# Kernel tuning notes

Measured on AMD Instinct MI355X. Metric: run time of the kernel, lower is better.

Reference implementation:

```python
import jax, jax.numpy as jnp
import numpy as np

D = 1024      # in_dim
HS = 64       # head_size
H = 16        # num_heads
B, S = 2, 2048


def setup_inputs() -> dict:
    key = jax.random.key(0)
    k1, k2, k3, k4, k5, k6 = jax.random.split(key, 6)
    scale = 1.0 / np.sqrt(D)
    x = jax.random.normal(k1, (B, S, D), dtype=jnp.float32)
    # Stacked per-head projection weights (torch Linear weight is [out,in];
    # random init so layout only needs to be consistent). query weight exists
    # in the torch module but is never used (source bug), so it is omitted.
    Wk = jax.random.normal(k2, (H, D, HS), dtype=jnp.float32) * scale
    Wv = jax.random.normal(k3, (H, D, HS), dtype=jnp.float32) * scale
    Wproj = jax.random.normal(k4, (H * HS, D), dtype=jnp.float32) * (1.0 / np.sqrt(H * HS))
    bproj = jax.random.normal(k5, (D,), dtype=jnp.float32) * 0.01
    return {"x": x, "Wk": Wk, "Wv": Wv, "Wproj": Wproj, "bproj": bproj}


def reference(x, Wk, Wv, Wproj, bproj):
    # Faithful to source: k = key(x); q = value(x); v = value(x)  (q == v, no softmax)
    k = jnp.einsum("bsd,hde->bhse", x, Wk)   # [B,H,S,HS]
    v = jnp.einsum("bsd,hde->bhse", x, Wv)   # [B,H,S,HS]
    q = v
    inv_sqrt = jnp.asarray(HS, x.dtype) ** -0.5
    wei = jnp.einsum("bhse,bhte->bhst", q, k) * inv_sqrt  # [B,H,S,S], unnormalized
    out = jnp.einsum("bhst,bhte->bhse", wei, v)            # [B,H,S,HS]
    # concat heads: [B,S,H*HS]
    out = jnp.transpose(out, (0, 2, 1, 3)).reshape(x.shape[0], x.shape[1], H * HS)
    return out @ Wproj + bproj  # [B,S,D]
```

## Files before the change

kernel.cpp:

```cpp
#include <hip/hip_runtime.h>

#define B_ 2
#define S_ 2048
#define D_ 1024
#define H_ 16
#define HS_ 64
#define HD_ 1024
#define BS_ (B_*S_)
#define KS_ 64
#define TP2_ 264

typedef __attribute__((ext_vector_type(8))) short short8_t;
typedef __attribute__((ext_vector_type(4))) float float4_t;

__device__ inline unsigned short f32_to_bf16(float f) {
  unsigned int u = __float_as_uint(f);
  u += 0x7FFF + ((u >> 16) & 1);
  return (unsigned short)(u >> 16);
}

__device__ inline void async_copy16(const void* g, void* lds) {
  __builtin_amdgcn_global_load_lds(
      (const __attribute__((address_space(1))) void*)g,
      (__attribute__((address_space(3))) void*)lds, 16, 0, 0);
}


__global__ __launch_bounds__(256) void prep_kernel(
    const float* __restrict__ x, const float* __restrict__ Wk,
    const float* __restrict__ Wv, unsigned short* __restrict__ xb,
    unsigned short* __restrict__ Wkvt) {
  const int blk = blockIdx.x;
  const int tid = threadIdx.x;
  __shared__ float lds[64][65];
  if (blk < 4096) {
    int idx = blk * 256 + tid;
    float4 v = ((const float4*)x)[idx];
    ushort4 o;
    o.x = f32_to_bf16(v.x); o.y = f32_to_bf16(v.y);
    o.z = f32_to_bf16(v.z); o.w = f32_to_bf16(v.w);
    ((ushort4*)xb)[idx] = o;
    return;
  }
  const int wblk = blk - 4096;
  const int h = wblk >> 4;
  const int d0 = (wblk & 15) * 64;
#pragma unroll
  for (int i = 0; i < 16; ++i) {
    int idx = tid + i * 256; int dd = idx >> 6, e = idx & 63;
    lds[e][dd] = Wk[((size_t)h * D_ + d0 + dd) * HS_ + e];
  }
  __syncthreads();
#pragma unroll
  for (int i = 0; i < 16; ++i) {
    int idx = tid + i * 256; int e = idx >> 6, dd = idx & 63;
    Wkvt[((size_t)h * 128 + e) * D_ + d0 + dd] = f32_to_bf16(lds[e][dd]);
  }
  __syncthreads();
#pragma unroll
  for (int i = 0; i < 16; ++i) {
    int idx = tid + i * 256; int dd = idx >> 6, e = idx & 63;
    lds[e][dd] = Wv[((size_t)h * D_ + d0 + dd) * HS_ + e];
  }
  __syncthreads();
#pragma unroll
  for (int i = 0; i < 16; ++i) {
    int idx = tid + i * 256; int e = idx >> 6, dd = idx & 63;
    Wkvt[((size_t)h * 128 + 64 + e) * D_ + d0 + dd] = f32_to_bf16(lds[e][dd]);
  }
}

__global__ __launch_bounds__(512) void kv_mfma_kernel(
    const unsigned short* __restrict__ xb,
    const unsigned short* __restrict__ Wkvt,
    unsigned short* __restrict__ Vb,
    float* __restrict__ Mpart) {
  const int blk = blockIdx.x;
  const int stile = blk & 15;
  const int h = blk >> 4;
  const int s0 = stile * 256;
  const int tid = threadIdx.x;
  const int lane = tid & 63;
  const int wid = tid >> 6;
  const int wm = wid >> 1, wn = wid & 1;
  const int quad = lane >> 4, l16 = lane & 15;
  const int srow8 = lane >> 3;
  const int sc8 = lane & 7;
  const int xa = l16 & 7;

  __shared__ __align__(16) unsigned char smem[98304];
  unsigned short* const A0 = (unsigned short*)smem;
  unsigned short* const B0 = (unsigned short*)(smem + 32768);
  unsigned short* const A1 = (unsigned short*)(smem + 49152);
  unsigned short* const B1 = (unsigned short*)(smem + 81920);
  unsigned short* const Ktl = (unsigned short*)smem;
  unsigned short* const Vtl = (unsigned short*)(smem + 64 * TP2_ * 2);

  float4_t acc[4][4];
  const float4_t fz = {0.f, 0.f, 0.f, 0.f};
#pragma unroll
  for (int i = 0; i < 4; ++i)
#pragma unroll
    for (int j = 0; j < 4; ++j) acc[i][j] = fz;

  auto stage_half = [&](int kt, unsigned short* Ad, unsigned short* Bd, int hf) {
    const int k0 = kt * KS_;
#pragma unroll
    for (int i = 0; i < 2; ++i) {
      int g = wid * 4 + hf * 2 + i;
      int r = g * 8 + srow8;
      int ch = (sc8 ^ (r & 7)) * 8;
      async_copy16(xb + (size_t)(s0 + r) * D_ + k0 + ch, Ad + g * 8 * KS_);
    }
    {
      int g = wid * 2 + hf;
      int r = g * 8 + srow8;
      int ch = (sc8 ^ (r & 7)) * 8;
      async_copy16(Wkvt + ((size_t)h * 128 + r) * D_ + k0 + ch, Bd + g * 8 * KS_);
    }
  };
  auto compute_phase = [&](const unsigned short* Ac, const unsigned short* Bc,
                           int ks) {
    short8_t a[4], b[4];
#pragma unroll
    for (int mi = 0; mi < 4; ++mi)
      a[mi] = *(const short8_t*)(Ac + (wm * 64 + mi * 16 + l16) * KS_ +
                                 ((ks * 4 + quad) ^ xa) * 8);
#pragma unroll
    for (int ni = 0; ni < 4; ++ni)
      b[ni] = *(const short8_t*)(Bc + (wn * 64 + ni * 16 + l16) * KS_ +
                                 ((ks * 4 + quad) ^ xa) * 8);
    __builtin_amdgcn_s_setprio(1);
#pragma unroll
    for (int mi = 0; mi < 4; ++mi)
#pragma unroll
      for (int ni = 0; ni < 4; ++ni)
        acc[mi][ni] = __builtin_amdgcn_mfma_f32_16x16x32_bf16(
            a[mi], b[ni], acc[mi][ni], 0, 0, 0);
    __builtin_amdgcn_s_setprio(0);
  };

  stage_half(0, A0, B0, 0);
  stage_half(0, A0, B0, 1);
  for (int t = 0; t < 16; ++t) {
    unsigned short* Ac = (t & 1) ? A1 : A0;
    unsigned short* Bc = (t & 1) ? B1 : B0;
    unsigned short* An = (t & 1) ? A0 : A1;
    unsigned short* Bn = (t & 1) ? B0 : B1;
    if (t < 15) {
      stage_half(t + 1, An, Bn, 0);
      asm volatile("s_waitcnt vmcnt(3)" ::: "memory");
    } else {
      asm volatile("s_waitcnt vmcnt(0)" ::: "memory");
    }
    __builtin_amdgcn_s_barrier();
    __builtin_amdgcn_sched_barrier(0);
    compute_phase(Ac, Bc, 0);
    __builtin_amdgcn_sched_barrier(0);
    __builtin_amdgcn_s_barrier();
    if (t < 15) stage_half(t + 1, An, Bn, 1);
    __builtin_amdgcn_s_barrier();
    __builtin_amdgcn_sched_barrier(0);
    compute_phase(Ac, Bc, 1);
    __builtin_amdgcn_sched_barrier(0);
    __builtin_amdgcn_s_barrier();
  }

  {
    unsigned short* dstT = (wn == 0) ? Ktl : Vtl;
#pragma unroll
    for (int mi = 0; mi < 4; ++mi)
#pragma unroll
      for (int ni = 0; ni < 4; ++ni) {
        int f = ni * 16 + l16;
        int sm = wm * 64 + mi * 16 + quad * 4;
        ushort4 o;
        o.x = f32_to_bf16(acc[mi][ni][0]);
        o.y = f32_to_bf16(acc[mi][ni][1]);
        o.z = f32_to_bf16(acc[mi][ni][2]);
        o.w = f32_to_bf16(acc[mi][ni][3]);
        *(ushort4*)&dstT[f * TP2_ + sm] = o;
      }
  }
  __syncthreads();

#pragma unroll
  for (int u = 0; u < 4; ++u) {
    int unit = tid + u * 512;
    int s = unit & 255;
    int ec = (unit >> 8) * 8;
    union { unsigned short u16[8]; uint4 v; } tv;
#pragma unroll
    for (int e = 0; e < 8; ++e) tv.u16[e] = Vtl[(ec + e) * TP2_ + s];
    *(uint4*)&Vb[(size_t)(s0 + s) * HD_ + h * 64 + ec] = tv.v;
  }

  {
    const int half = wid >> 2, fq = wid & 3;
    float4_t macc[4];
#pragma unroll
    for (int ni = 0; ni < 4; ++ni) macc[ni] = fz;
#pragma unroll
    for (int ss = 0; ss < 4; ++ss) {
      short8_t ka = *(const short8_t*)&Ktl[(fq * 16 + l16) * TP2_ +
                                           half * 128 + ss * 32 + quad * 8];
#pragma unroll
      for (int ni = 0; ni < 4; ++ni) {
        short8_t vv = *(const short8_t*)&Vtl[(ni * 16 + l16) * TP2_ +
                                             half * 128 + ss * 32 + quad * 8];
        macc[ni] = __builtin_amdgcn_mfma_f32_16x16x32_bf16(ka, vv, macc[ni], 0, 0, 0);
      }
    }
    float* mdst = Mpart + (((size_t)(stile * 2 + half)) * H_ + h) * 4096;
#pragma unroll
    for (int ni = 0; ni < 4; ++ni) {
      int e = ni * 16 + l16;
#pragma unroll
      for (int r = 0; r < 4; ++r) {
        int f = fq * 16 + quad * 4 + r;
        mdst[f * 64 + e] = macc[ni][r];
      }
    }
  }
}

__global__ __launch_bounds__(256) void m_reduce_kernel(
    const float* __restrict__ Mpart, float* __restrict__ M) {
  const int gid = blockIdx.x * 256 + threadIdx.x;
  const int e0 = gid * 4;
  const int bh = e0 >> 12;
  const int idx = e0 & 4095;
  const int b = bh >> 4, h = bh & 15;
  float4 s = {0.f, 0.f, 0.f, 0.f};
#pragma unroll
  for (int p = 0; p < 16; ++p) {
    const float4 v =
        *(const float4*)&Mpart[(((size_t)(b * 16 + p)) * H_ + h) * 4096 + idx];
    s.x += v.x; s.y += v.y; s.z += v.z; s.w += v.w;
  }
  s.x *= 0.125f; s.y *= 0.125f; s.z *= 0.125f; s.w *= 0.125f;
  *(float4*)&M[(size_t)bh * 4096 + idx] = s;
}

__global__ __launch_bounds__(256) void p_kernel(
    const float* __restrict__ M, const float* __restrict__ Wproj,
    unsigned short* __restrict__ Pt) {
  const int blk = blockIdx.x;
  const int dtile = blk & 15;
  const int h = (blk >> 4) & 15;
  const int b = blk >> 8;
  const int d0 = dtile * 64;
  const int tid = threadIdx.x;
  const int tx = tid & 15, ty = tid >> 4;
  __shared__ float Ms[64][68];
  __shared__ float Ws[64][68];
  const size_t mbase = ((size_t)(b * H_ + h)) * HS_ * HS_;
#pragma unroll
  for (int i = 0; i < 16; ++i) {
    int idx = tid + i * 256;
    int f = idx >> 6, e = idx & 63;
    Ms[e][f] = M[mbase + idx];
    Ws[f][e] = Wproj[(size_t)(h * HS_ + f) * D_ + d0 + e];
  }
  __syncthreads();
  float acc[4][4] = {};
#pragma unroll
  for (int kk = 0; kk < 64; ++kk) {
    const float4 a4 = *(const float4*)&Ms[kk][ty * 4];
    const float4 b4 = *(const float4*)&Ws[kk][tx * 4];
    const float a[4] = {a4.x, a4.y, a4.z, a4.w};
    const float bb[4] = {b4.x, b4.y, b4.z, b4.w};
#pragma unroll
    for (int i = 0; i < 4; ++i)
#pragma unroll
      for (int j = 0; j < 4; ++j) acc[i][j] += a[i] * bb[j];
  }
  __syncthreads();
#pragma unroll
  for (int i = 0; i < 4; ++i)
#pragma unroll
    for (int j = 0; j < 4; ++j)
      Ms[tx * 4 + j][ty * 4 + i] = acc[i][j];
  __syncthreads();
  {
    int c = tid >> 2, ch = tid & 3;
    unsigned short* dst = Pt + ((size_t)(b * D_ + d0 + c)) * HD_ + h * 64 + ch * 16;
#pragma unroll
    for (int e = 0; e < 16; ++e) dst[e] = f32_to_bf16(Ms[c][ch * 16 + e]);
  }
}

__global__ __launch_bounds__(512) void out_mfma_kernel(
    const unsigned short* __restrict__ Vb,
    const unsigned short* __restrict__ Pt,
    const float* __restrict__ bproj,
    float* __restrict__ out) {
  const int blk = blockIdx.x;
  const int ntile = blk & 7;
  const int stile = blk >> 3;
  const int s0 = stile * 128;
  const int n0 = ntile * 128;
  const int b = s0 >> 11;
  const int tid = threadIdx.x;
  const int lane = tid & 63;
  const int wid = tid >> 6;
  const int wm = wid & 1, wn = wid >> 1;
  const int quad = lane >> 4, l16 = lane & 15;
  const int srow8 = lane >> 3;
  const int sc8 = lane & 7;
  const int xa = l16 & 7;

  __shared__ __align__(16) unsigned char smem[65536];
  unsigned short* const A0 = (unsigned short*)smem;
  unsigned short* const B0 = (unsigned short*)(smem + 16384);
  unsigned short* const A1 = (unsigned short*)(smem + 32768);
  unsigned short* const B1 = (unsigned short*)(smem + 49152);

  float4_t acc[4][2];
  const float4_t fz = {0.f, 0.f, 0.f, 0.f};
#pragma unroll
  for (int i = 0; i < 4; ++i)
#pragma unroll
    for (int j = 0; j < 2; ++j) acc[i][j] = fz;

  const unsigned short* Bpanel = Pt + (size_t)b * D_ * HD_;
  auto stage_half = [&](int kt, unsigned short* Ad, unsigned short* Bd, int hf) {
    const int k0 = kt * KS_;
    {
      int g = wid * 2 + hf;
      int r = g * 8 + srow8;
      int ch = (sc8 ^ (r & 7)) * 8;
      async_copy16(Vb + (size_t)(s0 + r) * HD_ + k0 + ch, Ad + g * 8 * KS_);
    }
    {
      int g = wid * 2 + hf;
      int r = g * 8 + srow8;
      int ch = (sc8 ^ (r & 7)) * 8;
      async_copy16(Bpanel + (size_t)(n0 + r) * HD_ + k0 + ch, Bd + g * 8 * KS_);
    }
  };
  auto compute_phase = [&](const unsigned short* Ac, const unsigned short* Bc,
                           int ks) {
    short8_t a[4], bfr[2];
#pragma unroll
    for (int mi = 0; mi < 4; ++mi)
      a[mi] = *(const short8_t*)(Ac + (wm * 64 + mi * 16 + l16) * KS_ +
                                 ((ks * 4 + quad) ^ xa) * 8);
#pragma unroll
    for (int ni = 0; ni < 2; ++ni)
      bfr[ni] = *(const short8_t*)(Bc + (wn * 32 + ni * 16 + l16) * KS_ +
                                   ((ks * 4 + quad) ^ xa) * 8);
    __builtin_amdgcn_s_setprio(1);
#pragma unroll
    for (int mi = 0; mi < 4; ++mi)
#pragma unroll
      for (int ni = 0; ni < 2; ++ni)
        acc[mi][ni] = __builtin_amdgcn_mfma_f32_16x16x32_bf16(
            a[mi], bfr[ni], acc[mi][ni], 0, 0, 0);
    __builtin_amdgcn_s_setprio(0);
  };

  stage_half(0, A0, B0, 0);
  stage_half(0, A0, B0, 1);
  for (int t = 0; t < 16; ++t) {
    unsigned short* Ac = (t & 1) ? A1 : A0;
    unsigned short* Bc = (t & 1) ? B1 : B0;
    unsigned short* An = (t & 1) ? A0 : A1;
    unsigned short* Bn = (t & 1) ? B0 : B1;
    if (t < 15) {
      stage_half(t + 1, An, Bn, 0);
      asm volatile("s_waitcnt vmcnt(2)" ::: "memory");
    } else {
      asm volatile("s_waitcnt vmcnt(0)" ::: "memory");
    }
    __builtin_amdgcn_s_barrier();
    __builtin_amdgcn_sched_barrier(0);
    compute_phase(Ac, Bc, 0);
    __builtin_amdgcn_sched_barrier(0);
    __builtin_amdgcn_s_barrier();
    if (t < 15) stage_half(t + 1, An, Bn, 1);
    __builtin_amdgcn_s_barrier();
    __builtin_amdgcn_sched_barrier(0);
    compute_phase(Ac, Bc, 1);
    __builtin_amdgcn_sched_barrier(0);
    __builtin_amdgcn_s_barrier();
  }

#pragma unroll
  for (int ni = 0; ni < 2; ++ni) {
    int col = n0 + wn * 32 + ni * 16 + l16;
    float bias = bproj[col];
#pragma unroll
    for (int mi = 0; mi < 4; ++mi) {
      int rowb = s0 + wm * 64 + mi * 16 + quad * 4;
#pragma unroll
      for (int r = 0; r < 4; ++r)
        out[(size_t)(rowb + r) * D_ + col] = acc[mi][ni][r] + bias;
    }
  }
}

extern "C" void kernel_launch(void* const* d_in, const int* in_sizes, int n_in,
                              void* d_out, int out_size, void* d_ws, size_t ws_size,
                              hipStream_t stream) {
  const float* x = (const float*)d_in[0];
  const float* Wk = (const float*)d_in[1];
  const float* Wv = (const float*)d_in[2];
  const float* Wproj = (const float*)d_in[3];
  const float* bproj = (const float*)d_in[4];
  float* out = (float*)d_out;

  char* ws = (char*)d_ws;
  unsigned short* xb = (unsigned short*)ws;
  unsigned short* Wkvt = xb + (size_t)BS_ * D_;
  unsigned short* Vb = Wkvt + (size_t)H_ * 128 * D_;
  float* Mpart = (float*)(Vb + (size_t)BS_ * HD_);
  float* M = Mpart + (size_t)32 * H_ * 4096;
  unsigned short* Pt = (unsigned short*)(M + (size_t)B_ * H_ * 4096);

  prep_kernel<<<dim3(4096 + H_ * (D_ / 64)), dim3(256), 0, stream>>>(x, Wk, Wv, xb, Wkvt);
  kv_mfma_kernel<<<dim3(16 * H_), dim3(512), 0, stream>>>(xb, Wkvt, Vb, Mpart);
  m_reduce_kernel<<<dim3(128), dim3(256), 0, stream>>>(Mpart, M);
  p_kernel<<<dim3(B_ * H_ * (D_ / 64)), dim3(256), 0, stream>>>(M, Wproj, Pt);
  out_mfma_kernel<<<dim3(32 * 8), dim3(512), 0, stream>>>(Vb, Pt, bproj, out);
}
```

Baseline: 130.7 us.

## Triple-buffer LDS and interleave fragment reads with MFMA in the two GEMM kernels

The KV projection and output projection GEMMs move from double buffering in LDS to a three-slot ring with a prefetch distance of two k-tiles. Async global-to-LDS copies are split into smaller units and spread across the MFMA phases. Register fragments for the next sub-step are loaded from LDS while the current MFMAs run. The goal is to hide global load latency and LDS read latency behind matrix math, at the cost of more LDS per block (144KB and 96KB), which may lower occupancy, and more barriers per k-tile.

```diff
diff --git a/kernel.cpp b/kernel.cpp
--- a/kernel.cpp
+++ b/kernel.cpp
@@ -24,6 +24,15 @@
       (const __attribute__((address_space(1))) void*)g,
       (__attribute__((address_space(3))) void*)lds, 16, 0, 0);
 }
+
+#define WAITV6 asm volatile("s_waitcnt vmcnt(6)" ::: "memory")
+#define WAITV4 asm volatile("s_waitcnt vmcnt(4)" ::: "memory")
+#define WAITV0 asm volatile("s_waitcnt vmcnt(0)" ::: "memory")
+#define WAITL0 asm volatile("s_waitcnt lgkmcnt(0)" ::: "memory")
+#define BAR    __builtin_amdgcn_s_barrier()
+#define SCHEDB __builtin_amdgcn_sched_barrier(0)
+#define PRIO1  __builtin_amdgcn_s_setprio(1)
+#define PRIO0  __builtin_amdgcn_s_setprio(0)
 
 
 __global__ __launch_bounds__(256) void prep_kernel(
@@ -84,15 +93,9 @@
   const int wid = tid >> 6;
   const int wm = wid >> 1, wn = wid & 1;
   const int quad = lane >> 4, l16 = lane & 15;
-  const int srow8 = lane >> 3;
-  const int sc8 = lane & 7;
   const int xa = l16 & 7;
 
-  __shared__ __align__(16) unsigned char smem[98304];
-  unsigned short* const A0 = (unsigned short*)smem;
-  unsigned short* const B0 = (unsigned short*)(smem + 32768);
-  unsigned short* const A1 = (unsigned short*)(smem + 49152);
-  unsigned short* const B1 = (unsigned short*)(smem + 81920);
+  __shared__ __align__(16) unsigned char smem[147456];
   unsigned short* const Ktl = (unsigned short*)smem;
   unsigned short* const Vtl = (unsigned short*)(smem + 64 * TP2_ * 2);
 
@@ -103,68 +106,98 @@
 #pragma unroll
     for (int j = 0; j < 4; ++j) acc[i][j] = fz;
 
-  auto stage_half = [&](int kt, unsigned short* Ad, unsigned short* Bd, int hf) {
+  unsigned short* pc = (unsigned short*)(smem);
+  unsigned short* pn = (unsigned short*)(smem + 49152);
+  unsigned short* ps = (unsigned short*)(smem + 98304);
+
+  auto stageu = [&](unsigned short* slot, int kt, int u) {
     const int k0 = kt * KS_;
-#pragma unroll
-    for (int i = 0; i < 2; ++i) {
-      int g = wid * 4 + hf * 2 + i;
-      int r = g * 8 + srow8;
-      int ch = (sc8 ^ (r & 7)) * 8;
-      async_copy16(xb + (size_t)(s0 + r) * D_ + k0 + ch, Ad + g * 8 * KS_);
-    }
-    {
-      int g = wid * 2 + hf;
-      int r = g * 8 + srow8;
-      int ch = (sc8 ^ (r & 7)) * 8;
-      async_copy16(Wkvt + ((size_t)h * 128 + r) * D_ + k0 + ch, Bd + g * 8 * KS_);
-    }
-  };
-  auto compute_phase = [&](const unsigned short* Ac, const unsigned short* Bc,
-                           int ks) {
-    short8_t a[4], b[4];
-#pragma unroll
-    for (int mi = 0; mi < 4; ++mi)
-      a[mi] = *(const short8_t*)(Ac + (wm * 64 + mi * 16 + l16) * KS_ +
-                                 ((ks * 4 + quad) ^ xa) * 8);
-#pragma unroll
-    for (int ni = 0; ni < 4; ++ni)
-      b[ni] = *(const short8_t*)(Bc + (wn * 64 + ni * 16 + l16) * KS_ +
-                                 ((ks * 4 + quad) ^ xa) * 8);
-    __builtin_amdgcn_s_setprio(1);
-#pragma unroll
-    for (int mi = 0; mi < 4; ++mi)
-#pragma unroll
-      for (int ni = 0; ni < 4; ++ni)
-        acc[mi][ni] = __builtin_amdgcn_mfma_f32_16x16x32_bf16(
-            a[mi], b[ni], acc[mi][ni], 0, 0, 0);
-    __builtin_amdgcn_s_setprio(0);
-  };
-
-  stage_half(0, A0, B0, 0);
-  stage_half(0, A0, B0, 1);
-  for (int t = 0; t < 16; ++t) {
-    unsigned short* Ac = (t & 1) ? A1 : A0;
-    unsigned short* Bc = (t & 1) ? B1 : B0;
-    unsigned short* An = (t & 1) ? A0 : A1;
-    unsigned short* Bn = (t & 1) ? B0 : B1;
-    if (t < 15) {
-      stage_half(t + 1, An, Bn, 0);
-      asm volatile("s_waitcnt vmcnt(3)" ::: "memory");
+    if (u < 4) {
+      int rb = u * 64 + wid * 8;
+      int r = rb + (lane >> 3);
+      int ch = ((lane & 7) ^ (r & 7)) * 8;
+      async_copy16(xb + (size_t)(s0 + r) * D_ + k0 + ch, slot + rb * KS_);
     } else {
-      asm volatile("s_waitcnt vmcnt(0)" ::: "memory");
-    }
-    __builtin_amdgcn_s_barrier();
-    __builtin_amdgcn_sched_barrier(0);
-    compute_phase(Ac, Bc, 0);
-    __builtin_amdgcn_sched_barrier(0);
-    __builtin_amdgcn_s_barrier();
-    if (t < 15) stage_half(t + 1, An, Bn, 1);
-    __builtin_amdgcn_s_barrier();
-    __builtin_amdgcn_sched_barrier(0);
-    compute_phase(Ac, Bc, 1);
-    __builtin_amdgcn_sched_barrier(0);
-    __builtin_amdgcn_s_barrier();
-  }
+      int rb = (u - 4) * 64 + wid * 8;
+      int r = rb + (lane >> 3);
+      int ch = ((lane & 7) ^ (r & 7)) * 8;
+      async_copy16(Wkvt + ((size_t)h * 128 + r) * D_ + k0 + ch,
+                   slot + 16384 + rb * KS_);
+    }
+  };
+  auto rdA = [&](const unsigned short* P, int mi, int ks) {
+    return *(const short8_t*)(P + (wm * 64 + mi * 16 + l16) * KS_ +
+                              ((ks * 4 + quad) ^ xa) * 8);
+  };
+  auto rdB = [&](const unsigned short* P, int ni, int ks) {
+    return *(const short8_t*)(P + 16384 + (wn * 64 + ni * 16 + l16) * KS_ +
+                              ((ks * 4 + quad) ^ xa) * 8);
+  };
+
+  short8_t a0[4], a1[4], b0[4], b1[4];
+
+#pragma unroll
+  for (int u = 0; u < 6; ++u) stageu(pc, 0, u);
+#pragma unroll
+  for (int u = 0; u < 6; ++u) stageu(pn, 1, u);
+  WAITV6;
+  BAR;
+#pragma unroll
+  for (int mi = 0; mi < 4; ++mi) a0[mi] = rdA(pc, mi, 0);
+  b0[0] = rdB(pc, 0, 0); b0[1] = rdB(pc, 1, 0);
+
+  for (int kt = 0; kt < 16; ++kt) {
+    const bool st = (kt < 14);
+    if (st) { stageu(ps, kt + 2, 0); stageu(ps, kt + 2, 1); }
+    BAR; WAITL0; SCHEDB;
+    PRIO1;
+#pragma unroll
+    for (int mi = 0; mi < 4; ++mi) {
+      acc[mi][0] = __builtin_amdgcn_mfma_f32_16x16x32_bf16(a0[mi], b0[0], acc[mi][0], 0, 0, 0);
+      acc[mi][1] = __builtin_amdgcn_mfma_f32_16x16x32_bf16(a0[mi], b0[1], acc[mi][1], 0, 0, 0);
+    }
+    PRIO0;
+    b0[2] = rdB(pc, 2, 0); b0[3] = rdB(pc, 3, 0);
+    if (st) { stageu(ps, kt + 2, 2); stageu(ps, kt + 2, 3); }
+    BAR; WAITL0; SCHEDB;
+    PRIO1;
+#pragma unroll
+    for (int mi = 0; mi < 4; ++mi) {
+      acc[mi][2] = __builtin_amdgcn_mfma_f32_16x16x32_bf16(a0[mi], b0[2], acc[mi][2], 0, 0, 0);
+      acc[mi][3] = __builtin_amdgcn_mfma_f32_16x16x32_bf16(a0[mi], b0[3], acc[mi][3], 0, 0, 0);
+    }
+    PRIO0;
+#pragma unroll
+    for (int mi = 0; mi < 4; ++mi) a1[mi] = rdA(pc, mi, 1);
+    b1[0] = rdB(pc, 0, 1); b1[1] = rdB(pc, 1, 1);
+    if (st) stageu(ps, kt + 2, 4);
+    BAR; WAITL0; SCHEDB;
+    PRIO1;
+#pragma unroll
+    for (int mi = 0; mi < 4; ++mi) {
+      acc[mi][0] = __builtin_amdgcn_mfma_f32_16x16x32_bf16(a1[mi], b1[0], acc[mi][0], 0, 0, 0);
+      acc[mi][1] = __builtin_amdgcn_mfma_f32_16x16x32_bf16(a1[mi], b1[1], acc[mi][1], 0, 0, 0);
+    }
+    PRIO0;
+    b1[2] = rdB(pc, 2, 1); b1[3] = rdB(pc, 3, 1);
+    if (st) stageu(ps, kt + 2, 5);
+    if (kt < 14) { WAITV6; } else if (kt == 14) { WAITV0; }
+    BAR; WAITL0; SCHEDB;
+    PRIO1;
+#pragma unroll
+    for (int mi = 0; mi < 4; ++mi) {
+      acc[mi][2] = __builtin_amdgcn_mfma_f32_16x16x32_bf16(a1[mi], b1[2], acc[mi][2], 0, 0, 0);
+      acc[mi][3] = __builtin_amdgcn_mfma_f32_16x16x32_bf16(a1[mi], b1[3], acc[mi][3], 0, 0, 0);
+    }
+    PRIO0;
+    if (kt < 15) {
+#pragma unroll
+      for (int mi = 0; mi < 4; ++mi) a0[mi] = rdA(pn, mi, 0);
+      b0[0] = rdB(pn, 0, 0); b0[1] = rdB(pn, 1, 0);
+    }
+    unsigned short* t = pc; pc = pn; pn = ps; ps = t;
+  }
+  __syncthreads();
 
   {
     unsigned short* dstT = (wn == 0) ? Ktl : Vtl;
@@ -306,15 +339,9 @@
   const int wid = tid >> 6;
   const int wm = wid & 1, wn = wid >> 1;
   const int quad = lane >> 4, l16 = lane & 15;
-  const int srow8 = lane >> 3;
-  const int sc8 = lane & 7;
   const int xa = l16 & 7;
 
-  __shared__ __align__(16) unsigned char smem[65536];
-  unsigned short* const A0 = (unsigned short*)smem;
-  unsigned short* const B0 = (unsigned short*)(smem + 16384);
-  unsigned short* const A1 = (unsigned short*)(smem + 32768);
-  unsigned short* const B1 = (unsigned short*)(smem + 49152);
+  __shared__ __align__(16) unsigned char smem[98304];
 
   float4_t acc[4][2];
   const float4_t fz = {0.f, 0.f, 0.f, 0.f};
@@ -324,66 +351,77 @@
     for (int j = 0; j < 2; ++j) acc[i][j] = fz;
 
   const unsigned short* Bpanel = Pt + (size_t)b * D_ * HD_;
-  auto stage_half = [&](int kt, unsigned short* Ad, unsigned short* Bd, int hf) {
+
+  unsigned short* pc = (unsigned short*)(smem);
+  unsigned short* pn = (unsigned short*)(smem + 32768);
+  unsigned short* ps = (unsigned short*)(smem + 65536);
+
+  auto stageu = [&](unsigned short* slot, int kt, int u) {
     const int k0 = kt * KS_;
-    {
-      int g = wid * 2 + hf;
-      int r = g * 8 + srow8;
-      int ch = (sc8 ^ (r & 7)) * 8;
-      async_copy16(Vb + (size_t)(s0 + r) * HD_ + k0 + ch, Ad + g * 8 * KS_);
-    }
-    {
-      int g = wid * 2 + hf;
-      int r = g * 8 + srow8;
-      int ch = (sc8 ^ (r & 7)) * 8;
-      async_copy16(Bpanel + (size_t)(n0 + r) * HD_ + k0 + ch, Bd + g * 8 * KS_);
-    }
-  };
-  auto compute_phase = [&](const unsigned short* Ac, const unsigned short* Bc,
-                           int ks) {
-    short8_t a[4], bfr[2];
-#pragma unroll
-    for (int mi = 0; mi < 4; ++mi)
-      a[mi] = *(const short8_t*)(Ac + (wm * 64 + mi * 16 + l16) * KS_ +
-                                 ((ks * 4 + quad) ^ xa) * 8);
-#pragma unroll
-    for (int ni = 0; ni < 2; ++ni)
-      bfr[ni] = *(const short8_t*)(Bc + (wn * 32 + ni * 16 + l16) * KS_ +
-                                   ((ks * 4 + quad) ^ xa) * 8);
-    __builtin_amdgcn_s_setprio(1);
-#pragma unroll
-    for (int mi = 0; mi < 4; ++mi)
-#pragma unroll
-      for (int ni = 0; ni < 2; ++ni)
-        acc[mi][ni] = __builtin_amdgcn_mfma_f32_16x16x32_bf16(
-            a[mi], bfr[ni], acc[mi][ni], 0, 0, 0);
-    __builtin_amdgcn_s_setprio(0);
-  };
-
-  stage_half(0, A0, B0, 0);
-  stage_half(0, A0, B0, 1);
-  for (int t = 0; t < 16; ++t) {
-    unsigned short* Ac = (t & 1) ? A1 : A0;
-    unsigned short* Bc = (t & 1) ? B1 : B0;
-    unsigned short* An = (t & 1) ? A0 : A1;
-    unsigned short* Bn = (t & 1) ? B0 : B1;
-    if (t < 15) {
-      stage_half(t + 1, An, Bn, 0);
-      asm volatile("s_waitcnt vmcnt(2)" ::: "memory");
+    if (u < 2) {
+      int rb = u * 64 + wid * 8;
+      int r = rb + (lane >> 3);
+      int ch = ((lane & 7) ^ (r & 7)) * 8;
+      async_copy16(Vb + (size_t)(s0 + r) * HD_ + k0 + ch, slot + rb * KS_);
     } else {
-      asm volatile("s_waitcnt vmcnt(0)" ::: "memory");
-    }
-    __builtin_amdgcn_s_barrier();
-    __builtin_amdgcn_sched_barrier(0);
-    compute_phase(Ac, Bc, 0);
-    __builtin_amdgcn_sched_barrier(0);
-    __builtin_amdgcn_s_barrier();
-    if (t < 15) stage_half(t + 1, An, Bn, 1);
-    __builtin_amdgcn_s_barrier();
-    __builtin_amdgcn_sched_barrier(0);
-    compute_phase(Ac, Bc, 1);
-    __builtin_amdgcn_sched_barrier(0);
-    __builtin_amdgcn_s_barrier();
+      int rb = (u - 2) * 64 + wid * 8;
+      int r = rb + (lane >> 3);
+      int ch = ((lane & 7) ^ (r & 7)) * 8;
+      async_copy16(Bpanel + (size_t)(n0 + r) * HD_ + k0 + ch,
+                   slot + 8192 + rb * KS_);
+    }
+  };
+  auto rdA = [&](const unsigned short* P, int mi, int ks) {
+    return *(const short8_t*)(P + (wm * 64 + mi * 16 + l16) * KS_ +
+                              ((ks * 4 + quad) ^ xa) * 8);
+  };
+  auto rdB = [&](const unsigned short* P, int ni, int ks) {
+    return *(const short8_t*)(P + 8192 + (wn * 32 + ni * 16 + l16) * KS_ +
+                              ((ks * 4 + quad) ^ xa) * 8);
+  };
+
+  short8_t a0[4], a1[4], b0[2], b1[2];
+
+#pragma unroll
+  for (int u = 0; u < 4; ++u) stageu(pc, 0, u);
+#pragma unroll
+  for (int u = 0; u < 4; ++u) stageu(pn, 1, u);
+  WAITV4;
+  BAR;
+#pragma unroll
+  for (int mi = 0; mi < 4; ++mi) a0[mi] = rdA(pc, mi, 0);
+  b0[0] = rdB(pc, 0, 0); b0[1] = rdB(pc, 1, 0);
+
+  for (int kt = 0; kt < 16; ++kt) {
+    const bool st = (kt < 14);
+    if (st) { stageu(ps, kt + 2, 0); stageu(ps, kt + 2, 1); }
+    BAR; WAITL0; SCHEDB;
+    PRIO1;
+#pragma unroll
+    for (int mi = 0; mi < 4; ++mi) {
+      acc[mi][0] = __builtin_amdgcn_mfma_f32_16x16x32_bf16(a0[mi], b0[0], acc[mi][0], 0, 0, 0);
+      acc[mi][1] = __builtin_amdgcn_mfma_f32_16x16x32_bf16(a0[mi], b0[1], acc[mi][1], 0, 0, 0);
+    }
+    PRIO0;
+#pragma unroll
+    for (int mi = 0; mi < 4; ++mi) a1[mi] = rdA(pc, mi, 1);
+    b1[0] = rdB(pc, 0, 1); b1[1] = rdB(pc, 1, 1);
+    if (st) { stageu(ps, kt + 2, 2); stageu(ps, kt + 2, 3); }
+    if (kt < 14) { WAITV4; } else if (kt == 14) { WAITV0; }
+    BAR; WAITL0; SCHEDB;
+    PRIO1;
+#pragma unroll
+    for (int mi = 0; mi < 4; ++mi) {
+      acc[mi][0] = __builtin_amdgcn_mfma_f32_16x16x32_bf16(a1[mi], b1[0], acc[mi][0], 0, 0, 0);
+      acc[mi][1] = __builtin_amdgcn_mfma_f32_16x16x32_bf16(a1[mi], b1[1], acc[mi][1], 0, 0, 0);
+    }
+    PRIO0;
+    if (kt < 15) {
+#pragma unroll
+      for (int mi = 0; mi < 4; ++mi) a0[mi] = rdA(pn, mi, 0);
+      b0[0] = rdB(pn, 0, 0); b0[1] = rdB(pn, 1, 0);
+    }
+    unsigned short* t = pc; pc = pn; pn = ps; ps = t;
   }
 
 #pragma unroll
```

New measurement: 129.0 us. Within noise of the previous version (-1.3%).
